# Kernel optimization log

Measured on AMD Instinct MI355X. Metric: run time of the kernel, lower is better.

The kernel has to match this reference:

```python
import jax, jax.numpy as jnp
import numpy as np
from jax import lax

G, DIM, E, K, OC = 8, 32, 8, 2, 10  # groups, per-group channels, experts, top-k, out_channels


def setup_inputs() -> dict:
    key = jax.random.key(0)
    ks = jax.random.split(key, 6)
    B, L = 64, 4096
    x = jax.random.normal(ks[0], (B, G * DIM, L), dtype=jnp.float32)
    conv1_w = jax.random.normal(ks[1], (G * OC, DIM, 3), dtype=jnp.float32) * 0.05
    conv1_b = jax.random.normal(ks[2], (G * OC,), dtype=jnp.float32) * 0.05
    conv2_w = jax.random.normal(ks[3], (G * OC * E, OC, 1), dtype=jnp.float32) * 0.1
    conv2_b = jax.random.normal(ks[4], (G * OC * E,), dtype=jnp.float32) * 0.05
    w_gate = jax.random.normal(ks[5], (G, DIM * 5, E), dtype=jnp.float32) * 0.05
    return {"x": x, "conv1_w": conv1_w, "conv1_b": conv1_b,
            "conv2_w": conv2_w, "conv2_b": conv2_b, "w_gate": w_gate}


def _cv_squared(v):
    # torch .var() is unbiased (ddof=1)
    return jnp.var(v, ddof=1) / (jnp.mean(v) ** 2 + 1e-10)


def reference(x, conv1_w, conv1_b, conv2_w, conv2_b, w_gate):
    B, C, L = x.shape
    loss_coef = 0.01

    # ---- noisy_top_k_gating (eval path: no noise) per group, vectorized ----
    # gating input: last-6..last-1 timesteps of each group -> [B, G, DIM*5]
    gin = x.reshape(B, G, DIM, L)[:, :, :, -6:-1].reshape(B, G, DIM * 5)
    clean_logits = jnp.einsum('bgd,gde->bge', gin, w_gate)      # [B,G,E]
    probs = jax.nn.softmax(clean_logits, axis=-1)
    top_vals, top_idx = lax.top_k(probs, K)                      # [B,G,K]
    top_gates = top_vals / (jnp.sum(top_vals, axis=-1, keepdims=True) + 1e-6)
    onehot = jax.nn.one_hot(top_idx, E, dtype=probs.dtype)       # [B,G,K,E]
    gates = jnp.einsum('bgke,bgk->bge', onehot, top_gates)       # [B,G,E]

    load = jnp.sum(gates > 0, axis=0).astype(jnp.float32)        # [G,E]
    importance = jnp.sum(gates, axis=0)                          # [G,E]
    out_loss = loss_coef * (jax.vmap(_cv_squared)(importance).sum()
                            + jax.vmap(_cv_squared)(load).sum())

    # ---- per-group expert conv stacks as grouped conv1d ----
    dn = ('NCH', 'OIH', 'NCH')
    h = lax.conv_general_dilated(x, conv1_w, (1,), 'VALID',
                                 dimension_numbers=dn, feature_group_count=G)
    h = jnp.tanh(h + conv1_b[None, :, None])                     # [B, G*OC, L-2]
    o = lax.conv_general_dilated(h, conv2_w, (1,), 'VALID',
                                 dimension_numbers=dn, feature_group_count=G)
    o = o + conv2_b[None, :, None]                               # [B, G*OC*E, L']
    Lp = o.shape[-1]
    o = o.reshape(B, G, OC, E, Lp)  # channel c within group = d*E + e (matches torch reshape)

    # einsum 'BLDE,BE->BLD' then permute -> [B, G, OC, L']
    combine_features = jnp.einsum('bgdel,bge->bgdl', o, gates)
    gates_out = jnp.transpose(gates, (0, 2, 1))                  # [B, E, G]
    return combine_features, out_loss, gates_out
```

## Files before the change

### kernel.cpp

```cpp
#include <hip/hip_runtime.h>
#include <cmath>

#define B_    64
#define G_    8
#define DIM_  32
#define E_    8
#define OC_   10
#define LL    4096
#define LP    4094
#define COMBINE_SIZE (B_ * G_ * OC_ * LP)

__device__ __forceinline__ float fast_tanh(float v) {
    v = fminf(fmaxf(v, -12.f), 12.f);
    const float e = __expf(2.f * v);
    return 1.f - 2.f * __builtin_amdgcn_rcpf(e + 1.f);
}

__global__ void repack_kernel(const float* __restrict__ w1,
                              float* __restrict__ w1t) {
    const int i = blockIdx.x * 256 + threadIdx.x;
    if (i >= G_ * 32 * 30) return;
    const int g = i / 960, r = i - g * 960;
    const int d = r / 30,  s = r - d * 30;
    const int o = s / 3,   t = s - o * 3;
    w1t[g * 1024 + d * 32 + s] = w1[g * 960 + o * 96 + d * 3 + t];
}

__global__ void gate_kernel(const float* __restrict__ x,
                            const float* __restrict__ wg,
                            float* __restrict__ gws,
                            float* __restrict__ gout) {
    const int b   = blockIdx.x;
    const int tid = threadIdx.x;
    __shared__ float gin[G_ * 160];
    for (int i = tid; i < G_ * 160; i += 64) {
        int g = i / 160, r = i - g * 160;
        int d = r / 5,   t = r - d * 5;
        gin[i] = x[((size_t)b * (G_ * DIM_) + g * DIM_ + d) * LL + (LL - 6 + t)];
    }
    __syncthreads();
    const int g = tid >> 3, e = tid & 7;
    const float* gp = gin + g * 160;
    const float* wp = wg + (size_t)g * 160 * E_ + e;
    float acc = 0.f;
    for (int i = 0; i < 160; ++i) acc = fmaf(gp[i], wp[i * E_], acc);

    float m = acc;
    #pragma unroll
    for (int s = 4; s >= 1; s >>= 1) m = fmaxf(m, __shfl_xor(m, s));
    float p = expf(acc - m);
    float sum = p;
    #pragma unroll
    for (int s = 4; s >= 1; s >>= 1) sum += __shfl_xor(sum, s);
    p /= sum;

    float pv[8];
    const int base = tid & ~7;
    #pragma unroll
    for (int j = 0; j < 8; ++j) pv[j] = __shfl(p, base + j);
    int i1 = 0; float v1 = pv[0];
    #pragma unroll
    for (int j = 1; j < 8; ++j) if (pv[j] > v1) { v1 = pv[j]; i1 = j; }
    int i2 = -1; float v2 = -1.f;
    #pragma unroll
    for (int j = 0; j < 8; ++j) if (j != i1 && pv[j] > v2) { v2 = pv[j]; i2 = j; }
    const float denom = v1 + v2 + 1e-6f;
    const float gate = (e == i1) ? v1 / denom : ((e == i2) ? v2 / denom : 0.f);
    gws[(b * G_ + g) * E_ + e]   = gate;
    gout[b * (E_ * G_) + e * G_ + g] = gate;
}

__global__ void loss_kernel(const float* __restrict__ gws,
                            float* __restrict__ loss_out) {
    const int tid = threadIdx.x;
    float imp = 0.f, ld = 0.f;
    for (int b = 0; b < B_; ++b) {
        const float v = gws[b * 64 + tid];
        imp += v;
        ld  += (v > 0.f) ? 1.f : 0.f;
    }
    float si = imp, sl = ld;
    #pragma unroll
    for (int msk = 1; msk <= 4; msk <<= 1) { si += __shfl_xor(si, msk); sl += __shfl_xor(sl, msk); }
    const float mi = si * 0.125f, ml = sl * 0.125f;
    float di = imp - mi, dl = ld - ml;
    float vi = di * di, vl = dl * dl;
    #pragma unroll
    for (int msk = 1; msk <= 4; msk <<= 1) { vi += __shfl_xor(vi, msk); vl += __shfl_xor(vl, msk); }
    const float cvi = (vi / 7.f) / (mi * mi + 1e-10f);
    const float cvl = (vl / 7.f) / (ml * ml + 1e-10f);
    float c = ((tid & 7) == 0) ? (cvi + cvl) : 0.f;
    #pragma unroll
    for (int msk = 1; msk < 64; msk <<= 1) c += __shfl_xor(c, msk);
    if (tid == 0) *loss_out = 0.01f * c;
}

__global__ __launch_bounds__(256) void conv_kernel(
        const float* __restrict__ x,
        const float* __restrict__ w1t,
        const float* __restrict__ b1,
        const float* __restrict__ w2, const float* __restrict__ b2,
        const float* __restrict__ gws,
        float* __restrict__ out) {
    const int tid  = threadIdx.x;
    const int tile = blockIdx.x & 1;
    const int bg   = blockIdx.x >> 1;
    const int g    = bg & 7;
    const int b    = bg >> 3;

    __shared__ float weff[OC_ * OC_];
    __shared__ float beff[OC_];

    const float* gp = gws + bg * E_;
    if (tid < 100) {
        const int dd = tid / 10, j = tid - dd * 10;
        float s = 0.f;
        #pragma unroll
        for (int e = 0; e < 8; ++e)
            s = fmaf(gp[e], w2[(g * 80 + dd * 8 + e) * 10 + j], s);
        weff[tid] = s;
    } else if (tid < 110) {
        const int dd = tid - 100;
        float s = 0.f;
        #pragma unroll
        for (int e = 0; e < 8; ++e)
            s = fmaf(gp[e], b2[g * 80 + dd * 8 + e], s);
        beff[dd] = s;
    }
    __syncthreads();

    const int l = tile * 2048 + tid * 8;
    const float* xb  = x + ((size_t)b * 256 + g * 32) * LL + l;
    const float* wgt = w1t + g * 1024;
    const float* b1g = b1 + g * OC_;
    const bool hvalid = (l + 9 < LL);

    float acc[10][8];
    #pragma unroll
    for (int o = 0; o < 10; ++o) {
        const float bv = b1g[o];
        #pragma unroll
        for (int k = 0; k < 8; ++k) acc[o][k] = bv;
    }

#define XLOAD(P0, P1, PH, dd)                                                   \
    P0 = *reinterpret_cast<const float4*>(xb + (size_t)(dd) * LL);              \
    P1 = *reinterpret_cast<const float4*>(xb + (size_t)(dd) * LL + 4);          \
    PH = hvalid ? *reinterpret_cast<const float2*>(xb + (size_t)(dd) * LL + 8)  \
                : make_float2(0.f, 0.f);

#define XCOMP(P0, P1, PH, dd)                                                   \
    {                                                                           \
        const float xs[10] = {P0.x, P0.y, P0.z, P0.w,                           \
                              P1.x, P1.y, P1.z, P1.w, PH.x, PH.y};              \
        const float* wr = wgt + (size_t)(dd) * 32;                              \
        _Pragma("unroll")                                                       \
        for (int o = 0; o < 10; ++o) {                                          \
            const float w0 = wr[o * 3];                                         \
            const float wA = wr[o * 3 + 1];                                     \
            const float wB = wr[o * 3 + 2];                                     \
            _Pragma("unroll")                                                   \
            for (int k = 0; k < 8; ++k)                                         \
                acc[o][k] = fmaf(xs[k + 2], wB,                                 \
                            fmaf(xs[k + 1], wA,                                 \
                            fmaf(xs[k],     w0, acc[o][k])));                   \
        }                                                                       \
    }

    float4 a0, a1; float2 ah;
    float4 c0, c1; float2 ch;
    XLOAD(a0, a1, ah, 0)
    #pragma unroll 1
    for (int d = 0; d < 30; d += 2) {
        XLOAD(c0, c1, ch, d + 1)
        XCOMP(a0, a1, ah, d)
        XLOAD(a0, a1, ah, d + 2)
        XCOMP(c0, c1, ch, d + 1)
    }
    XLOAD(c0, c1, ch, 31)
    XCOMP(a0, a1, ah, 30)
    XCOMP(c0, c1, ch, 31)
#undef XLOAD
#undef XCOMP

    #pragma unroll
    for (int o = 0; o < 10; ++o)
        #pragma unroll
        for (int k = 0; k < 8; ++k)
            acc[o][k] = fast_tanh(acc[o][k]);

    float* ob = out + (size_t)bg * OC_ * LP + l;
    const bool full = (l + 8 <= LP);
    #pragma unroll
    for (int dd = 0; dd < 10; ++dd) {
        const float* wr = weff + dd * 10;
        float r[8];
        const float bv = beff[dd];
        #pragma unroll
        for (int k = 0; k < 8; ++k) r[k] = bv;
        #pragma unroll
        for (int j = 0; j < 10; ++j) {
            const float w = wr[j];
            #pragma unroll
            for (int k = 0; k < 8; ++k) r[k] = fmaf(acc[j][k], w, r[k]);
        }
        float* op = ob + (size_t)dd * LP;
        if (full) {
            *reinterpret_cast<float2*>(op)     = make_float2(r[0], r[1]);
            *reinterpret_cast<float2*>(op + 2) = make_float2(r[2], r[3]);
            *reinterpret_cast<float2*>(op + 4) = make_float2(r[4], r[5]);
            *reinterpret_cast<float2*>(op + 6) = make_float2(r[6], r[7]);
        } else {
            #pragma unroll
            for (int k = 0; k < 8; ++k)
                if (l + k < LP) op[k] = r[k];
        }
    }
}

extern "C" void kernel_launch(void* const* d_in, const int* in_sizes, int n_in,
                              void* d_out, int out_size, void* d_ws, size_t ws_size,
                              hipStream_t stream) {
    (void)in_sizes; (void)n_in; (void)out_size; (void)ws_size;
    const float* x  = (const float*)d_in[0];
    const float* w1 = (const float*)d_in[1];
    const float* b1 = (const float*)d_in[2];
    const float* w2 = (const float*)d_in[3];
    const float* b2 = (const float*)d_in[4];
    const float* wg = (const float*)d_in[5];
    float* out      = (float*)d_out;
    float* gws      = (float*)d_ws;
    float* w1t      = (float*)d_ws + B_ * G_ * E_;
    float* loss_out = out + COMBINE_SIZE;
    float* gout     = out + COMBINE_SIZE + 1;

    repack_kernel<<<(G_ * 32 * 30 + 255) / 256, 256, 0, stream>>>(w1, w1t);
    gate_kernel<<<B_, 64, 0, stream>>>(x, wg, gws, gout);
    loss_kernel<<<1, 64, 0, stream>>>(gws, loss_out);
    conv_kernel<<<B_ * G_ * 2, 256, 0, stream>>>(x, w1t, b1, w2, b2, gws, out);
}
```

Measured before the change: 112.6 us.

## Halve per-thread outputs, fetch conv halo via wave shuffles, raise occupancy

The conv kernel now computes 4 outputs per thread instead of 8 and launches four tiles per (batch, group) instead of two. The two-element conv halo comes from the neighbouring lane through __shfl_down, with only the last lane of each wave loading it from memory. This cuts redundant global loads and accumulator registers, and __launch_bounds__(256,8) is added to allow more waves per CU. The tanh input clamp is removed to save two instructions, which relies on __expf overflow saturating correctly. The price is more shuffle instructions per FMA and more blocks.

```diff
diff --git a/kernel.cpp b/kernel.cpp
--- a/kernel.cpp
+++ b/kernel.cpp
@@ -11,7 +11,6 @@
 #define COMBINE_SIZE (B_ * G_ * OC_ * LP)
 
 __device__ __forceinline__ float fast_tanh(float v) {
-    v = fminf(fmaxf(v, -12.f), 12.f);
     const float e = __expf(2.f * v);
     return 1.f - 2.f * __builtin_amdgcn_rcpf(e + 1.f);
 }
@@ -95,7 +94,7 @@
     if (tid == 0) *loss_out = 0.01f * c;
 }
 
-__global__ __launch_bounds__(256) void conv_kernel(
+__global__ __launch_bounds__(256, 8) void conv_kernel(
         const float* __restrict__ x,
         const float* __restrict__ w1t,
         const float* __restrict__ b1,
@@ -103,8 +102,9 @@
         const float* __restrict__ gws,
         float* __restrict__ out) {
     const int tid  = threadIdx.x;
-    const int tile = blockIdx.x & 1;
-    const int bg   = blockIdx.x >> 1;
+    const int lane = tid & 63;
+    const int tile = blockIdx.x & 3;
+    const int bg   = blockIdx.x >> 2;
     const int g    = bg & 7;
     const int b    = bg >> 3;
 
@@ -129,30 +129,33 @@
     }
     __syncthreads();
 
-    const int l = tile * 2048 + tid * 8;
+    const int l = tile * 1024 + tid * 4;
     const float* xb  = x + ((size_t)b * 256 + g * 32) * LL + l;
     const float* wgt = w1t + g * 1024;
     const float* b1g = b1 + g * OC_;
-    const bool hvalid = (l + 9 < LL);
-
-    float acc[10][8];
+    const bool l63  = (lane == 63);
+    const bool hval = l63 && (l + 5 < LL);
+
+    float acc[10][4];
     #pragma unroll
     for (int o = 0; o < 10; ++o) {
         const float bv = b1g[o];
         #pragma unroll
-        for (int k = 0; k < 8; ++k) acc[o][k] = bv;
-    }
-
-#define XLOAD(P0, P1, PH, dd)                                                   \
-    P0 = *reinterpret_cast<const float4*>(xb + (size_t)(dd) * LL);              \
-    P1 = *reinterpret_cast<const float4*>(xb + (size_t)(dd) * LL + 4);          \
-    PH = hvalid ? *reinterpret_cast<const float2*>(xb + (size_t)(dd) * LL + 8)  \
-                : make_float2(0.f, 0.f);
-
-#define XCOMP(P0, P1, PH, dd)                                                   \
+        for (int k = 0; k < 4; ++k) acc[o][k] = bv;
+    }
+
+#define XLOAD(P, H, dd)                                                         \
+    P = *reinterpret_cast<const float4*>(xb + (size_t)(dd) * LL);               \
+    H = make_float2(0.f, 0.f);                                                  \
+    if (hval) H = *reinterpret_cast<const float2*>(xb + (size_t)(dd) * LL + 4);
+
+#define XCOMP(P, H, dd)                                                         \
     {                                                                           \
-        const float xs[10] = {P0.x, P0.y, P0.z, P0.w,                           \
-                              P1.x, P1.y, P1.z, P1.w, PH.x, PH.y};              \
+        float h0 = __shfl_down(P.x, 1);                                         \
+        float h1 = __shfl_down(P.y, 1);                                         \
+        h0 = l63 ? H.x : h0;                                                    \
+        h1 = l63 ? H.y : h1;                                                    \
+        const float xs[6] = {P.x, P.y, P.z, P.w, h0, h1};                       \
         const float* wr = wgt + (size_t)(dd) * 32;                              \
         _Pragma("unroll")                                                       \
         for (int o = 0; o < 10; ++o) {                                          \
@@ -160,59 +163,57 @@
             const float wA = wr[o * 3 + 1];                                     \
             const float wB = wr[o * 3 + 2];                                     \
             _Pragma("unroll")                                                   \
-            for (int k = 0; k < 8; ++k)                                         \
+            for (int k = 0; k < 4; ++k)                                         \
                 acc[o][k] = fmaf(xs[k + 2], wB,                                 \
                             fmaf(xs[k + 1], wA,                                 \
                             fmaf(xs[k],     w0, acc[o][k])));                   \
         }                                                                       \
     }
 
-    float4 a0, a1; float2 ah;
-    float4 c0, c1; float2 ch;
-    XLOAD(a0, a1, ah, 0)
+    float4 a0; float2 ah;
+    float4 c0; float2 ch;
+    XLOAD(a0, ah, 0)
     #pragma unroll 1
     for (int d = 0; d < 30; d += 2) {
-        XLOAD(c0, c1, ch, d + 1)
-        XCOMP(a0, a1, ah, d)
-        XLOAD(a0, a1, ah, d + 2)
-        XCOMP(c0, c1, ch, d + 1)
-    }
-    XLOAD(c0, c1, ch, 31)
-    XCOMP(a0, a1, ah, 30)
-    XCOMP(c0, c1, ch, 31)
+        XLOAD(c0, ch, d + 1)
+        XCOMP(a0, ah, d)
+        XLOAD(a0, ah, d + 2)
+        XCOMP(c0, ch, d + 1)
+    }
+    XLOAD(c0, ch, 31)
+    XCOMP(a0, ah, 30)
+    XCOMP(c0, ch, 31)
 #undef XLOAD
 #undef XCOMP
 
     #pragma unroll
     for (int o = 0; o < 10; ++o)
         #pragma unroll
-        for (int k = 0; k < 8; ++k)
+        for (int k = 0; k < 4; ++k)
             acc[o][k] = fast_tanh(acc[o][k]);
 
     float* ob = out + (size_t)bg * OC_ * LP + l;
-    const bool full = (l + 8 <= LP);
+    const bool full = (l + 4 <= LP);
     #pragma unroll
     for (int dd = 0; dd < 10; ++dd) {
         const float* wr = weff + dd * 10;
-        float r[8];
+        float r[4];
         const float bv = beff[dd];
         #pragma unroll
-        for (int k = 0; k < 8; ++k) r[k] = bv;
+        for (int k = 0; k < 4; ++k) r[k] = bv;
         #pragma unroll
         for (int j = 0; j < 10; ++j) {
             const float w = wr[j];
             #pragma unroll
-            for (int k = 0; k < 8; ++k) r[k] = fmaf(acc[j][k], w, r[k]);
+            for (int k = 0; k < 4; ++k) r[k] = fmaf(acc[j][k], w, r[k]);
         }
         float* op = ob + (size_t)dd * LP;
         if (full) {
             *reinterpret_cast<float2*>(op)     = make_float2(r[0], r[1]);
             *reinterpret_cast<float2*>(op + 2) = make_float2(r[2], r[3]);
-            *reinterpret_cast<float2*>(op + 4) = make_float2(r[4], r[5]);
-            *reinterpret_cast<float2*>(op + 6) = make_float2(r[6], r[7]);
         } else {
             #pragma unroll
-            for (int k = 0; k < 8; ++k)
+            for (int k = 0; k < 4; ++k)
                 if (l + k < LP) op[k] = r[k];
         }
     }
@@ -237,5 +238,5 @@
     repack_kernel<<<(G_ * 32 * 30 + 255) / 256, 256, 0, stream>>>(w1, w1t);
     gate_kernel<<<B_, 64, 0, stream>>>(x, wg, gws, gout);
     loss_kernel<<<1, 64, 0, stream>>>(gws, loss_out);
-    conv_kernel<<<B_ * G_ * 2, 256, 0, stream>>>(x, w1t, b1, w2, b2, gws, out);
-}
+    conv_kernel<<<B_ * G_ * 4, 256, 0, stream>>>(x, w1t, b1, w2, b2, gws, out);
+}
```

Measured after the change: 158.1 us. 1.4x slower.

## Stage x rows through double-buffered LDS with one block per batch-group

Applied to the files above, without the earlier changes.

Each block now covers a whole (batch, group) row span with 512 threads instead of two 256-thread tiles. Input rows are loaded once into a padded, double-buffered LDS array, and neighbouring elements for the 3-tap conv are read from LDS. This removes the overlapping halo global loads and prefetches the next channel while the current one is computed. The change also drops the tanh input clamp and tightens the launch bounds. In exchange it adds 32 block-wide barriers, extra LDS traffic and possibly misaligned 128-bit LDS reads, since the padded per-thread stride of 9 floats is not 16-byte aligned.

```diff
diff --git a/kernel.cpp b/kernel.cpp
--- a/kernel.cpp
+++ b/kernel.cpp
@@ -9,9 +9,9 @@
 #define LL    4096
 #define LP    4094
 #define COMBINE_SIZE (B_ * G_ * OC_ * LP)
+#define LDSN  4616
 
 __device__ __forceinline__ float fast_tanh(float v) {
-    v = fminf(fmaxf(v, -12.f), 12.f);
     const float e = __expf(2.f * v);
     return 1.f - 2.f * __builtin_amdgcn_rcpf(e + 1.f);
 }
@@ -95,19 +95,18 @@
     if (tid == 0) *loss_out = 0.01f * c;
 }
 
-__global__ __launch_bounds__(256) void conv_kernel(
+__global__ __launch_bounds__(512, 4) void conv_kernel(
         const float* __restrict__ x,
         const float* __restrict__ w1t,
         const float* __restrict__ b1,
         const float* __restrict__ w2, const float* __restrict__ b2,
         const float* __restrict__ gws,
         float* __restrict__ out) {
-    const int tid  = threadIdx.x;
-    const int tile = blockIdx.x & 1;
-    const int bg   = blockIdx.x >> 1;
-    const int g    = bg & 7;
-    const int b    = bg >> 3;
-
+    const int tid = threadIdx.x;
+    const int bg  = blockIdx.x;
+    const int g   = bg & 7;
+
+    __shared__ float xsb[2][LDSN];
     __shared__ float weff[OC_ * OC_];
     __shared__ float beff[OC_];
 
@@ -126,14 +125,14 @@
         for (int e = 0; e < 8; ++e)
             s = fmaf(gp[e], b2[g * 80 + dd * 8 + e], s);
         beff[dd] = s;
-    }
-    __syncthreads();
-
-    const int l = tile * 2048 + tid * 8;
-    const float* xb  = x + ((size_t)b * 256 + g * 32) * LL + l;
-    const float* wgt = w1t + g * 1024;
-    const float* b1g = b1 + g * OC_;
-    const bool hvalid = (l + 9 < LL);
+    } else if (tid >= 128 && tid < 144) {
+        const int i = tid - 128;
+        xsb[i >> 3][4608 + (i & 7)] = 0.f;
+    }
+
+    const float* xrow = x + ((size_t)bg * 32) * LL;
+    const float* wgt  = w1t + g * 1024;
+    const float* b1g  = b1 + g * OC_;
 
     float acc[10][8];
     #pragma unroll
@@ -143,45 +142,47 @@
         for (int k = 0; k < 8; ++k) acc[o][k] = bv;
     }
 
-#define XLOAD(P0, P1, PH, dd)                                                   \
-    P0 = *reinterpret_cast<const float4*>(xb + (size_t)(dd) * LL);              \
-    P1 = *reinterpret_cast<const float4*>(xb + (size_t)(dd) * LL + 4);          \
-    PH = hvalid ? *reinterpret_cast<const float2*>(xb + (size_t)(dd) * LL + 8)  \
-                : make_float2(0.f, 0.f);
-
-#define XCOMP(P0, P1, PH, dd)                                                   \
-    {                                                                           \
-        const float xs[10] = {P0.x, P0.y, P0.z, P0.w,                           \
-                              P1.x, P1.y, P1.z, P1.w, PH.x, PH.y};              \
-        const float* wr = wgt + (size_t)(dd) * 32;                              \
-        _Pragma("unroll")                                                       \
-        for (int o = 0; o < 10; ++o) {                                          \
-            const float w0 = wr[o * 3];                                         \
-            const float wA = wr[o * 3 + 1];                                     \
-            const float wB = wr[o * 3 + 2];                                     \
-            _Pragma("unroll")                                                   \
-            for (int k = 0; k < 8; ++k)                                         \
-                acc[o][k] = fmaf(xs[k + 2], wB,                                 \
-                            fmaf(xs[k + 1], wA,                                 \
-                            fmaf(xs[k],     w0, acc[o][k])));                   \
-        }                                                                       \
-    }
-
-    float4 a0, a1; float2 ah;
-    float4 c0, c1; float2 ch;
-    XLOAD(a0, a1, ah, 0)
+    const int fo = tid * 8;
+    const int pb = tid * 9;
+
+    float4 ra = *reinterpret_cast<const float4*>(xrow + fo);
+    float4 rb = *reinterpret_cast<const float4*>(xrow + fo + 4);
+    *reinterpret_cast<float4*>(&xsb[0][pb])     = ra;
+    *reinterpret_cast<float4*>(&xsb[0][pb + 4]) = rb;
+    __syncthreads();
+
     #pragma unroll 1
-    for (int d = 0; d < 30; d += 2) {
-        XLOAD(c0, c1, ch, d + 1)
-        XCOMP(a0, a1, ah, d)
-        XLOAD(a0, a1, ah, d + 2)
-        XCOMP(c0, c1, ch, d + 1)
-    }
-    XLOAD(c0, c1, ch, 31)
-    XCOMP(a0, a1, ah, 30)
-    XCOMP(c0, c1, ch, 31)
-#undef XLOAD
-#undef XCOMP
+    for (int d = 0; d < 32; ++d) {
+        const int cur = d & 1;
+        if (d < 31) {
+            const float* xr = xrow + (size_t)(d + 1) * LL + fo;
+            ra = *reinterpret_cast<const float4*>(xr);
+            rb = *reinterpret_cast<const float4*>(xr + 4);
+        }
+        const float* sb = xsb[cur];
+        float xw[10];
+        *reinterpret_cast<float4*>(&xw[0]) = *reinterpret_cast<const float4*>(&sb[pb]);
+        *reinterpret_cast<float4*>(&xw[4]) = *reinterpret_cast<const float4*>(&sb[pb + 4]);
+        xw[8] = sb[pb + 9];
+        xw[9] = sb[pb + 10];
+        const float* wr = wgt + d * 32;
+        #pragma unroll
+        for (int o = 0; o < 10; ++o) {
+            const float w0 = wr[o * 3];
+            const float wA = wr[o * 3 + 1];
+            const float wB = wr[o * 3 + 2];
+            #pragma unroll
+            for (int k = 0; k < 8; ++k)
+                acc[o][k] = fmaf(xw[k + 2], wB,
+                            fmaf(xw[k + 1], wA,
+                            fmaf(xw[k],     w0, acc[o][k])));
+        }
+        if (d < 31) {
+            *reinterpret_cast<float4*>(&xsb[cur ^ 1][pb])     = ra;
+            *reinterpret_cast<float4*>(&xsb[cur ^ 1][pb + 4]) = rb;
+        }
+        __syncthreads();
+    }
 
     #pragma unroll
     for (int o = 0; o < 10; ++o)
@@ -189,8 +190,8 @@
         for (int k = 0; k < 8; ++k)
             acc[o][k] = fast_tanh(acc[o][k]);
 
-    float* ob = out + (size_t)bg * OC_ * LP + l;
-    const bool full = (l + 8 <= LP);
+    float* ob = out + (size_t)bg * OC_ * LP + fo;
+    const bool full = (fo + 8 <= LP);
     #pragma unroll
     for (int dd = 0; dd < 10; ++dd) {
         const float* wr = weff + dd * 10;
@@ -213,7 +214,7 @@
         } else {
             #pragma unroll
             for (int k = 0; k < 8; ++k)
-                if (l + k < LP) op[k] = r[k];
+                if (fo + k < LP) op[k] = r[k];
         }
     }
 }
@@ -237,5 +238,5 @@
     repack_kernel<<<(G_ * 32 * 30 + 255) / 256, 256, 0, stream>>>(w1, w1t);
     gate_kernel<<<B_, 64, 0, stream>>>(x, wg, gws, gout);
     loss_kernel<<<1, 64, 0, stream>>>(gws, loss_out);
-    conv_kernel<<<B_ * G_ * 2, 256, 0, stream>>>(x, w1t, b1, w2, b2, gws, out);
-}
+    conv_kernel<<<B_ * G_, 512, 0, stream>>>(x, w1t, b1, w2, b2, gws, out);
+}
```

New measurement: 110.8 us. Within noise of the previous version (-1.6%).

## Stage input rows through swizzled LDS ring with async global_load_lds

Applied to the files above, without the earlier changes.

The conv kernel now uses one 512-thread block per (batch, group) and covers the full sequence, where it previously used two 256-thread tiles. Each of the 32 input channel rows is streamed into a 4-slot LDS ring with direct global-to-LDS loads, three rows ahead, guarded by vmcnt waits and barriers. Threads read their overlapping 10-element windows from LDS through an XOR swizzle to avoid bank conflicts, replacing the redundant per-thread halo loads from global memory. The change also drops the tanh input clamp. This adds a barrier per row and halves the grid to 512 blocks, which may reduce occupancy.

```diff
diff --git a/kernel.cpp b/kernel.cpp
--- a/kernel.cpp
+++ b/kernel.cpp
@@ -3,17 +3,21 @@
 
 #define B_    64
 #define G_    8
-#define DIM_  32
 #define E_    8
 #define OC_   10
 #define LL    4096
 #define LP    4094
 #define COMBINE_SIZE (B_ * G_ * OC_ * LP)
+#define SLOT  4104
 
 __device__ __forceinline__ float fast_tanh(float v) {
-    v = fminf(fmaxf(v, -12.f), 12.f);
     const float e = __expf(2.f * v);
     return 1.f - 2.f * __builtin_amdgcn_rcpf(e + 1.f);
+}
+
+__device__ __forceinline__ int gswz(int g) {
+    const int c = g & 63;
+    return (g & ~63) | (c ^ (c >> 3));
 }
 
 __global__ void repack_kernel(const float* __restrict__ w1,
@@ -36,7 +40,7 @@
     for (int i = tid; i < G_ * 160; i += 64) {
         int g = i / 160, r = i - g * 160;
         int d = r / 5,   t = r - d * 5;
-        gin[i] = x[((size_t)b * (G_ * DIM_) + g * DIM_ + d) * LL + (LL - 6 + t)];
+        gin[i] = x[((size_t)b * 256 + g * 32 + d) * LL + (LL - 6 + t)];
     }
     __syncthreads();
     const int g = tid >> 3, e = tid & 7;
@@ -95,7 +99,7 @@
     if (tid == 0) *loss_out = 0.01f * c;
 }
 
-__global__ __launch_bounds__(256) void conv_kernel(
+__global__ __launch_bounds__(512) void conv_kernel(
         const float* __restrict__ x,
         const float* __restrict__ w1t,
         const float* __restrict__ b1,
@@ -103,13 +107,16 @@
         const float* __restrict__ gws,
         float* __restrict__ out) {
     const int tid  = threadIdx.x;
-    const int tile = blockIdx.x & 1;
-    const int bg   = blockIdx.x >> 1;
+    const int lane = tid & 63;
+    const int wq   = tid >> 6;
+    const int bg   = blockIdx.x;
     const int g    = bg & 7;
-    const int b    = bg >> 3;
-
+
+    __shared__ float ring[4][SLOT];
     __shared__ float weff[OC_ * OC_];
     __shared__ float beff[OC_];
+
+    if (tid < 32) ring[tid >> 3][4096 + (tid & 7)] = 0.f;
 
     const float* gp = gws + bg * E_;
     if (tid < 100) {
@@ -129,11 +136,25 @@
     }
     __syncthreads();
 
-    const int l = tile * 2048 + tid * 8;
-    const float* xb  = x + ((size_t)b * 256 + g * 32) * LL + l;
-    const float* wgt = w1t + g * 1024;
-    const float* b1g = b1 + g * OC_;
-    const bool hvalid = (l + 9 < LL);
+    const float* xrow = x + (size_t)bg * 32 * LL;
+    const float* wgt  = w1t + g * 1024;
+    const float* b1g  = b1 + g * OC_;
+
+    const int sl = (lane ^ (lane >> 3)) * 4;
+
+#define STAGE(r)                                                              \
+    {                                                                         \
+        const float* gb = xrow + (size_t)(r) * LL + (wq * 2) * 256;           \
+        float* lb = &ring[(r) & 3][(wq * 2) * 256];                           \
+        __builtin_amdgcn_global_load_lds(                                     \
+            (const __attribute__((address_space(1))) void*)(gb + sl),         \
+            (__attribute__((address_space(3))) void*)lb, 16, 0, 0);           \
+        __builtin_amdgcn_global_load_lds(                                     \
+            (const __attribute__((address_space(1))) void*)(gb + 256 + sl),   \
+            (__attribute__((address_space(3))) void*)(lb + 256), 16, 0, 0);   \
+    }
+
+#define WAITV(n) asm volatile("s_waitcnt vmcnt(" #n ")" ::: "memory");
 
     float acc[10][8];
     #pragma unroll
@@ -143,45 +164,53 @@
         for (int k = 0; k < 8; ++k) acc[o][k] = bv;
     }
 
-#define XLOAD(P0, P1, PH, dd)                                                   \
-    P0 = *reinterpret_cast<const float4*>(xb + (size_t)(dd) * LL);              \
-    P1 = *reinterpret_cast<const float4*>(xb + (size_t)(dd) * LL + 4);          \
-    PH = hvalid ? *reinterpret_cast<const float2*>(xb + (size_t)(dd) * LL + 8)  \
-                : make_float2(0.f, 0.f);
-
-#define XCOMP(P0, P1, PH, dd)                                                   \
-    {                                                                           \
-        const float xs[10] = {P0.x, P0.y, P0.z, P0.w,                           \
-                              P1.x, P1.y, P1.z, P1.w, PH.x, PH.y};              \
-        const float* wr = wgt + (size_t)(dd) * 32;                              \
-        _Pragma("unroll")                                                       \
-        for (int o = 0; o < 10; ++o) {                                          \
-            const float w0 = wr[o * 3];                                         \
-            const float wA = wr[o * 3 + 1];                                     \
-            const float wB = wr[o * 3 + 2];                                     \
-            _Pragma("unroll")                                                   \
-            for (int k = 0; k < 8; ++k)                                         \
-                acc[o][k] = fmaf(xs[k + 2], wB,                                 \
-                            fmaf(xs[k + 1], wA,                                 \
-                            fmaf(xs[k],     w0, acc[o][k])));                   \
-        }                                                                       \
-    }
-
-    float4 a0, a1; float2 ah;
-    float4 c0, c1; float2 ch;
-    XLOAD(a0, a1, ah, 0)
+    const int p1 = gswz(tid * 2) * 4;
+    const int p2 = gswz(tid * 2 + 1) * 4;
+    const int p3 = gswz(tid * 2 + 2) * 4;
+
+#define COMPROW(dd)                                                           \
+    {                                                                         \
+        const float* sb = ring[(dd) & 3];                                     \
+        float xw[10];                                                         \
+        *reinterpret_cast<float4*>(&xw[0]) =                                  \
+            *reinterpret_cast<const float4*>(sb + p1);                        \
+        *reinterpret_cast<float4*>(&xw[4]) =                                  \
+            *reinterpret_cast<const float4*>(sb + p2);                        \
+        const float2 t2 = *reinterpret_cast<const float2*>(sb + p3);          \
+        xw[8] = t2.x; xw[9] = t2.y;                                           \
+        const float* wr = wgt + (dd) * 32;                                    \
+        _Pragma("unroll")                                                     \
+        for (int o = 0; o < 10; ++o) {                                        \
+            const float w0 = wr[o * 3];                                       \
+            const float wA = wr[o * 3 + 1];                                   \
+            const float wB = wr[o * 3 + 2];                                   \
+            _Pragma("unroll")                                                 \
+            for (int k = 0; k < 8; ++k)                                       \
+                acc[o][k] = fmaf(xw[k + 2], wB,                               \
+                            fmaf(xw[k + 1], wA,                              \
+                            fmaf(xw[k],     w0, acc[o][k])));                 \
+        }                                                                     \
+    }
+
+    STAGE(0) STAGE(1) STAGE(2)
+
     #pragma unroll 1
-    for (int d = 0; d < 30; d += 2) {
-        XLOAD(c0, c1, ch, d + 1)
-        XCOMP(a0, a1, ah, d)
-        XLOAD(a0, a1, ah, d + 2)
-        XCOMP(c0, c1, ch, d + 1)
-    }
-    XLOAD(c0, c1, ch, 31)
-    XCOMP(a0, a1, ah, 30)
-    XCOMP(c0, c1, ch, 31)
-#undef XLOAD
-#undef XCOMP
+    for (int d = 0; d < 30; ++d) {
+        WAITV(4)
+        __builtin_amdgcn_s_barrier();
+        if (d < 29) STAGE(d + 3)
+        COMPROW(d)
+    }
+    WAITV(2)
+    __builtin_amdgcn_s_barrier();
+    COMPROW(30)
+    WAITV(0)
+    __builtin_amdgcn_s_barrier();
+    COMPROW(31)
+
+#undef STAGE
+#undef WAITV
+#undef COMPROW
 
     #pragma unroll
     for (int o = 0; o < 10; ++o)
@@ -189,6 +218,7 @@
         for (int k = 0; k < 8; ++k)
             acc[o][k] = fast_tanh(acc[o][k]);
 
+    const int l = tid * 8;
     float* ob = out + (size_t)bg * OC_ * LP + l;
     const bool full = (l + 8 <= LP);
     #pragma unroll
@@ -237,5 +267,5 @@
     repack_kernel<<<(G_ * 32 * 30 + 255) / 256, 256, 0, stream>>>(w1, w1t);
     gate_kernel<<<B_, 64, 0, stream>>>(x, wg, gws, gout);
     loss_kernel<<<1, 64, 0, stream>>>(gws, loss_out);
-    conv_kernel<<<B_ * G_ * 2, 256, 0, stream>>>(x, w1t, b1, w2, b2, gws, out);
-}
+    conv_kernel<<<B_ * G_, 512, 0, stream>>>(x, w1t, b1, w2, b2, gws, out);
+}
```

Measured after the change: 106.5 us. -5.4%, faster.
